# Performance work log

Hardware: AMD Instinct MI355X
Metric: run time of the kernel (lower is better)

The kernel has to match this reference:

```python
import jax, jax.numpy as jnp
import numpy as np

C0, C1 = 16, 16
V, E = 100000, 1600000
TWO_PI = 6.2831853


def setup_inputs() -> dict:
    key = jax.random.key(0)
    ks = jax.random.split(key, 12)
    s0 = 1.0 / np.sqrt(C0)
    s1 = 1.0 / np.sqrt(C1)
    return {
        "x": jax.random.normal(ks[0], (V, C0 + 2 * C1), dtype=jnp.float32),
        "edge_index": jax.random.randint(ks[1], (2, E), 0, V, dtype=jnp.int64),
        "angles": jax.random.uniform(ks[2], (E,), dtype=jnp.float32) * TWO_PI,
        "transporters": jax.random.uniform(ks[3], (E,), dtype=jnp.float32) * TWO_PI,
        "e1": jax.random.normal(ks[4], (V, 3), dtype=jnp.float32),
        "e2": jax.random.normal(ks[5], (V, 3), dtype=jnp.float32),
        # mag head (out rho0): self rho0->rho0, neigh rho0->rho0 (const), neigh rho1->rho0 (2 basis coeffs/chan)
        "w_self0": jax.random.normal(ks[6], (C0,), dtype=jnp.float32) * s0,
        "w_n00": jax.random.normal(ks[7], (C0,), dtype=jnp.float32) * s0,
        "w_n10": jax.random.normal(ks[8], (C1, 2), dtype=jnp.float32) * s1,
        # tangent head (out rho1): self rho1->rho1 {I,J}, neigh rho0->rho1 (2), neigh rho1->rho1 (4)
        "w_self11": jax.random.normal(ks[9], (C1, 2), dtype=jnp.float32) * s1,
        "w_n01": jax.random.normal(ks[10], (C0, 2), dtype=jnp.float32) * s0,
        "w_n11": jax.random.normal(ks[11], (C1, 4), dtype=jnp.float32) * s1,
    }


def _gem_head(x, edge_index, angles, transporters,
              w_self0, w_n00, w_n10, w_self11, w_n01, w_n11):
    """Gauge-equivariant message passing (GEM-CNN style).
    Returns (tangent_coeffs (V,2), mag (V,))."""
    nV = x.shape[0]
    x0 = x[:, :C0]                       # (V, C0) scalar (rho0) channels
    x1 = x[:, C0:].reshape(nV, C1, 2)    # (V, C1, 2) vector (rho1) channels
    src, dst = edge_index[0], edge_index[1]

    # gather + parallel transport of rho1 features (rotate by transporter angle g)
    cg, sg = jnp.cos(transporters)[:, None], jnp.sin(transporters)[:, None]
    x1s = x1[src]                        # (E, C1, 2)
    u1 = cg * x1s[..., 0] - sg * x1s[..., 1]
    u2 = sg * x1s[..., 0] + cg * x1s[..., 1]
    x0s = x0[src]                        # (E, C0)

    ct, st = jnp.cos(angles)[:, None], jnp.sin(angles)[:, None]
    c2t, s2t = jnp.cos(2.0 * angles)[:, None], jnp.sin(2.0 * angles)[:, None]

    # ---- rho0 output (magnitude) messages ----
    # rho0->rho0: constant kernel; rho1->rho0: basis (cos,sin) and (-sin,cos)
    m0 = x0s @ w_n00 \
        + (ct * u1 + st * u2) @ w_n10[:, 0] \
        + (-st * u1 + ct * u2) @ w_n10[:, 1]          # (E,)

    # ---- rho1 output (tangent) messages ----
    # rho0->rho1: K = a*(cos,sin)^T + b*(-sin,cos)^T
    sa = x0s @ w_n01[:, 0]
    sb = x0s @ w_n01[:, 1]
    mv1 = sa * ct[:, 0] - sb * st[:, 0]
    mv2 = sa * st[:, 0] + sb * ct[:, 0]
    # rho1->rho1: basis {I, J, Refl(2t), J*Refl(2t)}
    p, q, r, s = w_n11[:, 0], w_n11[:, 1], w_n11[:, 2], w_n11[:, 3]
    r1 = c2t * u1 + s2t * u2
    r2 = s2t * u1 - c2t * u2
    mv1 = mv1 + u1 @ p - u2 @ q + r1 @ r - r2 @ s
    mv2 = mv2 + u2 @ p + u1 @ q + r2 @ r + r1 @ s

    # ---- mean aggregation over incoming edges ----
    deg = jax.ops.segment_sum(jnp.ones_like(m0), dst, num_segments=nV)
    denom = jnp.maximum(deg, 1.0)
    mag = jax.ops.segment_sum(m0, dst, num_segments=nV) / denom
    agg1 = jax.ops.segment_sum(mv1, dst, num_segments=nV) / denom
    agg2 = jax.ops.segment_sum(mv2, dst, num_segments=nV) / denom

    # ---- self kernels (Schur-allowed blocks only) ----
    mag = mag + x0 @ w_self0
    sa_, sb_ = w_self11[:, 0], w_self11[:, 1]
    t1 = agg1 + x1[..., 0] @ sa_ - x1[..., 1] @ sb_
    t2 = agg2 + x1[..., 1] @ sa_ + x1[..., 0] @ sb_
    return jnp.stack([t1, t2], axis=-1), mag


def reference(x, edge_index, angles, transporters, e1, e2,
              w_self0, w_n00, w_n10, w_self11, w_n01, w_n11):
    tangent, mag = _gem_head(x, edge_index, angles, transporters,
                             w_self0, w_n00, w_n10, w_self11, w_n01, w_n11)
    mag_scale = jax.nn.sigmoid(mag)[:, None] * 2.0      # (V,1)
    wss_3d = tangent[:, 0:1] * e1 + tangent[:, 1:2] * e2  # (V,3)
    return wss_3d * mag_scale
```

## Files before the change

### kernel.cpp

```cpp
#include <hip/hip_runtime.h>
#include <math.h>


#define VB 256
#define VB_SHIFT 8
#define MAXNB 400
#define CHUNK 3125
#define NCHUNK 512
#define BIGT 1024
#define CAP_SHIFT 13
#define CAP (1 << CAP_SHIFT)
#define FIXS 131072.0f
#define FIXSI (1.0f / 131072.0f)
#define BIASI (1 << 22)

typedef unsigned int uint32;
typedef unsigned long long uint64;

static __device__ __forceinline__ uint32 f2bf(float f) {
    uint32 u = __float_as_uint(f);
    return (u + 0x7FFFu + ((u >> 16) & 1u)) >> 16;
}
static __device__ __forceinline__ uint32 pack2(float lo, float hi) {
    return f2bf(lo) | (f2bf(hi) << 16);
}
static __device__ __forceinline__ float bf_lo(uint32 u) {
    return __uint_as_float(u << 16);
}
static __device__ __forceinline__ float bf_hi(uint32 u) {
    return __uint_as_float(u & 0xFFFF0000u);
}

__global__ __launch_bounds__(256)
void precompute_kernel(const float* __restrict__ x,
                       const float* __restrict__ w_self0,
                       const float* __restrict__ w_n00,
                       const float* __restrict__ w_n10,
                       const float* __restrict__ w_self11,
                       const float* __restrict__ w_n01,
                       const float* __restrict__ w_n11,
                       uint32* __restrict__ table,
                       float* __restrict__ selfbuf,
                       int* __restrict__ fill,
                       int V, int NB) {
    __shared__ float stage[256 * 49];
    int tid = threadIdx.x;
    if (blockIdx.x == 0) {
        for (int i = tid; i < NB; i += 256) fill[i] = 0;
    }
    int v0 = blockIdx.x * 256;
    int nv = min(256, V - v0);
    if (nv <= 0) return;
    {
        const float4* x4 = (const float4*)(x + (size_t)v0 * 48);
        int n4 = nv * 12;
        for (int j = tid; j < n4; j += 256) {
            float4 f = x4[j];
            float* dp = stage + (j / 12) * 49 + (j % 12) * 4;
            dp[0] = f.x; dp[1] = f.y; dp[2] = f.z; dp[3] = f.w;
        }
    }
    __syncthreads();
    if (tid >= nv) return;
    int v = v0 + tid;
    const float* xr = stage + tid * 49;
    float d00 = 0.f, aw0 = 0.f, bw0 = 0.f, aw1 = 0.f, bw1 = 0.f;
    float d01a = 0.f, d01b = 0.f;
    float aP = 0.f, bP = 0.f, aQ = 0.f, bQ = 0.f;
    float aR = 0.f, bR = 0.f, aS = 0.f, bS = 0.f;
    float selfmag = 0.f, t1s = 0.f, t2s = 0.f;
#pragma unroll
    for (int i = 0; i < 16; ++i) {
        float x0 = xr[i];
        float a  = xr[16 + 2 * i];
        float b  = xr[17 + 2 * i];
        d00     += x0 * w_n00[i];
        selfmag += x0 * w_self0[i];
        d01a    += x0 * w_n01[i * 2 + 0];
        d01b    += x0 * w_n01[i * 2 + 1];
        float w0 = w_n10[i * 2 + 0], w1 = w_n10[i * 2 + 1];
        aw0 += a * w0;  bw0 += b * w0;
        aw1 += a * w1;  bw1 += b * w1;
        float p = w_n11[i * 4 + 0], q = w_n11[i * 4 + 1];
        float r = w_n11[i * 4 + 2], s = w_n11[i * 4 + 3];
        aP += a * p;  bP += b * p;
        aQ += a * q;  bQ += b * q;
        aR += a * r;  bR += b * r;
        aS += a * s;  bS += b * s;
        float sa_ = w_self11[i * 2 + 0], sb_ = w_self11[i * 2 + 1];
        t1s += a * sa_ - b * sb_;
        t2s += b * sa_ + a * sb_;
    }
    uint4 w0, w1;
    w0.x = pack2(d00, aw0);  w0.y = pack2(bw0, aw1);
    w0.z = pack2(bw1, d01a); w0.w = pack2(d01b, aP);
    w1.x = pack2(bP, aQ);    w1.y = pack2(bQ, aR);
    w1.z = pack2(bR, aS);    w1.w = pack2(bS, 0.f);
    uint4* tp = (uint4*)(table + (size_t)v * 8);
    tp[0] = w0;  tp[1] = w1;
    float* sf = selfbuf + (size_t)v * 4;
    sf[0] = selfmag; sf[1] = t1s; sf[2] = t2s; sf[3] = 0.f;
}

__global__ __launch_bounds__(BIGT)
void scatter_kernel(const int* __restrict__ src,
                    const int* __restrict__ dst,
                    const float* __restrict__ angles,
                    const float* __restrict__ transporters,
                    const uint32* __restrict__ table,
                    int* __restrict__ fill,
                    uint2* __restrict__ payload,
                    int E, int NB) {
    __shared__ int cnt_l[MAXNB];
    __shared__ int exoff_l[MAXNB];
    __shared__ int slot_l[MAXNB];
    __shared__ int wsum[16];
    __shared__ uint32 tw_src[CHUNK];
    __shared__ uint32 tw_ang[CHUNK];
    __shared__ uint32 tw_tr[CHUNK];
    __shared__ unsigned short tw_bin[CHUNK];

    int b = blockIdx.x;
    int lo = b * CHUNK;
    int hi = min(E, lo + CHUNK);
    int nloc = hi - lo;
    int tid = threadIdx.x;
    int lane = tid & 63;
    int wv = tid >> 6;

    for (int i = tid; i < NB; i += BIGT) cnt_l[i] = 0;
    __syncthreads();

    for (int e = lo + tid; e < hi; e += BIGT)
        atomicAdd(&cnt_l[dst[e] >> VB_SHIFT], 1);
    __syncthreads();

    int c = (tid < NB) ? cnt_l[tid] : 0;
    int rsv = 0;
    if (tid < NB && c > 0) rsv = atomicAdd(&fill[tid], c);

    int incl = c;
#pragma unroll
    for (int d = 1; d < 64; d <<= 1) {
        int n = __shfl_up(incl, d);
        if (lane >= d) incl += n;
    }
    if (lane == 63) wsum[wv] = incl;
    __syncthreads();
    if (tid < 16) {
        int wval = wsum[tid], winc = wval;
#pragma unroll
        for (int d = 1; d < 16; d <<= 1) {
            int n = __shfl_up(winc, d);
            if (lane >= d) winc += n;
        }
        wsum[tid] = winc - wval;
    }
    __syncthreads();
    if (tid < NB) {
        int ex = incl - c + wsum[wv];
        exoff_l[tid] = ex;
        cnt_l[tid] = ex;
        slot_l[tid] = (tid << CAP_SHIFT) + rsv;
    }
    __syncthreads();

    for (int e = lo + tid; e < hi; e += BIGT) {
        int d = dst[e];
        int bin = d >> VB_SHIFT;
        uint32 dl = (uint32)(d & (VB - 1));
        int pos = atomicAdd(&cnt_l[bin], 1);
        tw_src[pos] = (uint32)src[e] | (dl << 17);
        tw_ang[pos] = __float_as_uint(angles[e]);
        tw_tr[pos]  = __float_as_uint(transporters[e]);
        tw_bin[pos] = (unsigned short)bin;
    }
    __syncthreads();

    for (int k = tid; k < nloc; k += BIGT) {
        int bin = (int)tw_bin[k];
        uint32 w0i = tw_src[k];
        int s  = (int)(w0i & 0x1FFFFu);
        int dl = (int)(w0i >> 17);
        float ang = __uint_as_float(tw_ang[k]);
        float trv = __uint_as_float(tw_tr[k]);
        float st = __sinf(ang), ct = __cosf(ang);
        float sg = __sinf(trv), cg = __cosf(trv);
        float c2t = ct * ct - st * st;
        float s2t = 2.0f * st * ct;

        const uint4* tp = (const uint4*)(table + (size_t)s * 8);
        uint4 W0 = tp[0], W1 = tp[1];
        float d00 = bf_lo(W0.x), aw0 = bf_hi(W0.x);
        float bw0 = bf_lo(W0.y), aw1 = bf_hi(W0.y);
        float bw1 = bf_lo(W0.z), d01a = bf_hi(W0.z);
        float d01b = bf_lo(W0.w), aP = bf_hi(W0.w);
        float bP = bf_lo(W1.x), aQ = bf_hi(W1.x);
        float bQ = bf_lo(W1.y), aR = bf_hi(W1.y);
        float bR = bf_lo(W1.z), aS = bf_hi(W1.z);
        float bS = bf_lo(W1.w);

        float u1w0 = cg * aw0 - sg * bw0, u2w0 = sg * aw0 + cg * bw0;
        float u1w1 = cg * aw1 - sg * bw1, u2w1 = sg * aw1 + cg * bw1;
        float m0 = d00 + ct * u1w0 + st * u2w0 - st * u1w1 + ct * u2w1;

        float u1p = cg * aP - sg * bP, u2p = sg * aP + cg * bP;
        float u1q = cg * aQ - sg * bQ, u2q = sg * aQ + cg * bQ;
        float u1r = cg * aR - sg * bR, u2r = sg * aR + cg * bR;
        float u1s = cg * aS - sg * bS, u2s = sg * aS + cg * bS;

        float mv1 = d01a * ct - d01b * st
                  + u1p - u2q
                  + c2t * u1r + s2t * u2r
                  - (s2t * u1s - c2t * u2s);
        float mv2 = d01a * st + d01b * ct
                  + u2p + u1q
                  + s2t * u1r - c2t * u2r
                  + c2t * u1s + s2t * u2s;

        uint2 pl;
        pl.x = pack2(m0, mv1);
        pl.y = f2bf(mv2) | ((uint32)dl << 16);
        int g = slot_l[bin] + (k - exoff_l[bin]);
        if (g < ((bin + 1) << CAP_SHIFT))
            payload[g] = pl;
    }
}

__global__ __launch_bounds__(BIGT)
void bucket_kernel(const uint2* __restrict__ payload,
                   const int* __restrict__ fill,
                   const float* __restrict__ selfbuf,
                   const float* __restrict__ e1,
                   const float* __restrict__ e2,
                   float* __restrict__ out,
                   int V) {
    __shared__ uint64 acc[8][VB * 2];
    int bin = blockIdx.x;
    int tid = threadIdx.x;
    for (int i = tid; i < 8 * VB * 2; i += BIGT) ((uint64*)acc)[i] = 0ULL;
    __syncthreads();

    int n = min(fill[bin], CAP);
    const uint2* pp = payload + ((size_t)bin << CAP_SHIFT);
    uint64* myacc = acc[tid >> 7];
    for (int k = tid; k < n; k += BIGT) {
        uint2 pl = pp[k];
        float m0  = bf_lo(pl.x);
        float mv1 = bf_hi(pl.x);
        float mv2 = bf_lo(pl.y);
        int dl = (int)(pl.y >> 16);
        int m0f  = __float2int_rn(m0  * FIXS);
        int mv1f = __float2int_rn(mv1 * FIXS);
        int mv2f = __float2int_rn(mv2 * FIXS);
        uint64 pa = (uint64)(uint32)(m0f + BIASI)
                  | ((uint64)(uint32)mv1f << 32);
        uint64 pb = (uint64)(uint32)(mv2f + BIASI)
                  | (1ULL << 32);
        atomicAdd(&myacc[dl * 2 + 0], pa);
        atomicAdd(&myacc[dl * 2 + 1], pb);
    }
    __syncthreads();
    if (tid < VB) {
        int v = bin * VB + tid;
        if (v < V) {
            int cnt = 0, m0s = 0, mv1s = 0, mv2s = 0;
#pragma unroll
            for (int w = 0; w < 8; ++w) {
                uint64 a = acc[w][tid * 2 + 0];
                uint64 b = acc[w][tid * 2 + 1];
                uint32 nw = (uint32)(b >> 32);
                cnt  += (int)nw;
                m0s  += (int)((uint32)a - nw * (uint32)BIASI);
                mv1s += (int)(a >> 32);
                mv2s += (int)((uint32)b - nw * (uint32)BIASI);
            }
            float A0 = (float)m0s  * FIXSI;
            float A1 = (float)mv1s * FIXSI;
            float A2 = (float)mv2s * FIXSI;
            float inv = 1.0f / fmaxf((float)cnt, 1.0f);
            const float* sf = selfbuf + (size_t)v * 4;
            float mag = A0 * inv + sf[0];
            float t1  = A1 * inv + sf[1];
            float t2  = A2 * inv + sf[2];
            float scale = 2.0f / (1.0f + expf(-mag));
            float e1x = e1[v * 3 + 0], e1y = e1[v * 3 + 1], e1z = e1[v * 3 + 2];
            float e2x = e2[v * 3 + 0], e2y = e2[v * 3 + 1], e2z = e2[v * 3 + 2];
            out[v * 3 + 0] = (t1 * e1x + t2 * e2x) * scale;
            out[v * 3 + 1] = (t1 * e1y + t2 * e2y) * scale;
            out[v * 3 + 2] = (t1 * e1z + t2 * e2z) * scale;
        }
    }
}

extern "C" void kernel_launch(void* const* d_in, const int* in_sizes, int n_in,
                              void* d_out, int out_size, void* d_ws, size_t ws_size,
                              hipStream_t stream) {
    const float* x            = (const float*)d_in[0];
    const int*   edge_index   = (const int*)d_in[1];
    const float* angles       = (const float*)d_in[2];
    const float* transporters = (const float*)d_in[3];
    const float* e1           = (const float*)d_in[4];
    const float* e2           = (const float*)d_in[5];
    const float* w_self0      = (const float*)d_in[6];
    const float* w_n00        = (const float*)d_in[7];
    const float* w_n10        = (const float*)d_in[8];
    const float* w_self11     = (const float*)d_in[9];
    const float* w_n01        = (const float*)d_in[10];
    const float* w_n11        = (const float*)d_in[11];
    float* out = (float*)d_out;

    int V = in_sizes[0] / 48;
    int E = in_sizes[2];
    const int* src = edge_index;
    const int* dst = edge_index + E;

    int NB = (V + VB - 1) / VB;
    int nchunk = (E + CHUNK - 1) / CHUNK;

    char* p = (char*)d_ws;
    int* fill      = (int*)p;     p += (size_t)MAXNB * 4;
    uint32* table  = (uint32*)p;  p += (size_t)V * 8 * 4;
    float* selfbuf = (float*)p;   p += (size_t)V * 4 * 4;
    p = (char*)(((uintptr_t)p + 63) & ~(uintptr_t)63);
    uint2* payload = (uint2*)p;

    int gv = (V + 255) / 256;

    precompute_kernel<<<gv, 256, 0, stream>>>(
        x, w_self0, w_n00, w_n10, w_self11, w_n01, w_n11,
        table, selfbuf, fill, V, NB);
    scatter_kernel<<<nchunk, BIGT, 0, stream>>>(src, dst, angles,
                                                transporters, table,
                                                fill, payload, E, NB);
    bucket_kernel<<<NB, BIGT, 0, stream>>>(payload, fill, selfbuf,
                                           e1, e2, out, V);
}
```

Measured before the change: 138.3 us.

## Replace bucketed scatter with direct global 64-bit atomic accumulation per vertex

Removes the binning scatter kernel, the bf16 payload buffer and the LDS bucket reduction. Each edge now computes its message and does two packed fixed-point 64-bit atomicAdds straight into a per-vertex global accumulator, which precompute zeroes and a small finalize kernel reads. This drops the payload write/read round trip and the LDS sorting, at the cost of many contended global atomics over random destinations. It also removes the bf16 rounding of messages and the per-bin capacity limit.

```diff
diff --git a/kernel.cpp b/kernel.cpp
--- a/kernel.cpp
+++ b/kernel.cpp
@@ -2,14 +2,7 @@
 #include <math.h>
 
 
-#define VB 256
-#define VB_SHIFT 8
 #define MAXNB 400
-#define CHUNK 3125
-#define NCHUNK 512
-#define BIGT 1024
-#define CAP_SHIFT 13
-#define CAP (1 << CAP_SHIFT)
 #define FIXS 131072.0f
 #define FIXSI (1.0f / 131072.0f)
 #define BIASI (1 << 22)
@@ -41,16 +34,17 @@
                        const float* __restrict__ w_n11,
                        uint32* __restrict__ table,
                        float* __restrict__ selfbuf,
-                       int* __restrict__ fill,
-                       int V, int NB) {
+                       uint64* __restrict__ acc,
+                       int V) {
     __shared__ float stage[256 * 49];
     int tid = threadIdx.x;
-    if (blockIdx.x == 0) {
-        for (int i = tid; i < NB; i += 256) fill[i] = 0;
-    }
     int v0 = blockIdx.x * 256;
     int nv = min(256, V - v0);
     if (nv <= 0) return;
+    if (tid < nv) {
+        uint4 z = {0u, 0u, 0u, 0u};
+        *((uint4*)(acc + (size_t)(v0 + tid) * 2)) = z;
+    }
     {
         const float4* x4 = (const float4*)(x + (size_t)v0 * 48);
         int n4 = nv * 12;
@@ -102,88 +96,21 @@
     sf[0] = selfmag; sf[1] = t1s; sf[2] = t2s; sf[3] = 0.f;
 }
 
-__global__ __launch_bounds__(BIGT)
-void scatter_kernel(const int* __restrict__ src,
-                    const int* __restrict__ dst,
-                    const float* __restrict__ angles,
-                    const float* __restrict__ transporters,
-                    const uint32* __restrict__ table,
-                    int* __restrict__ fill,
-                    uint2* __restrict__ payload,
-                    int E, int NB) {
-    __shared__ int cnt_l[MAXNB];
-    __shared__ int exoff_l[MAXNB];
-    __shared__ int slot_l[MAXNB];
-    __shared__ int wsum[16];
-    __shared__ uint32 tw_src[CHUNK];
-    __shared__ uint32 tw_ang[CHUNK];
-    __shared__ uint32 tw_tr[CHUNK];
-    __shared__ unsigned short tw_bin[CHUNK];
-
-    int b = blockIdx.x;
-    int lo = b * CHUNK;
-    int hi = min(E, lo + CHUNK);
-    int nloc = hi - lo;
-    int tid = threadIdx.x;
-    int lane = tid & 63;
-    int wv = tid >> 6;
-
-    for (int i = tid; i < NB; i += BIGT) cnt_l[i] = 0;
-    __syncthreads();
-
-    for (int e = lo + tid; e < hi; e += BIGT)
-        atomicAdd(&cnt_l[dst[e] >> VB_SHIFT], 1);
-    __syncthreads();
-
-    int c = (tid < NB) ? cnt_l[tid] : 0;
-    int rsv = 0;
-    if (tid < NB && c > 0) rsv = atomicAdd(&fill[tid], c);
-
-    int incl = c;
-#pragma unroll
-    for (int d = 1; d < 64; d <<= 1) {
-        int n = __shfl_up(incl, d);
-        if (lane >= d) incl += n;
-    }
-    if (lane == 63) wsum[wv] = incl;
-    __syncthreads();
-    if (tid < 16) {
-        int wval = wsum[tid], winc = wval;
-#pragma unroll
-        for (int d = 1; d < 16; d <<= 1) {
-            int n = __shfl_up(winc, d);
-            if (lane >= d) winc += n;
-        }
-        wsum[tid] = winc - wval;
-    }
-    __syncthreads();
-    if (tid < NB) {
-        int ex = incl - c + wsum[wv];
-        exoff_l[tid] = ex;
-        cnt_l[tid] = ex;
-        slot_l[tid] = (tid << CAP_SHIFT) + rsv;
-    }
-    __syncthreads();
-
-    for (int e = lo + tid; e < hi; e += BIGT) {
+__global__ __launch_bounds__(256)
+void edge_kernel(const int* __restrict__ src,
+                 const int* __restrict__ dst,
+                 const float* __restrict__ angles,
+                 const float* __restrict__ transporters,
+                 const uint32* __restrict__ table,
+                 uint64* __restrict__ acc,
+                 int E) {
+    int i0 = blockIdx.x * 256 + threadIdx.x;
+    int stride = gridDim.x * 256;
+    for (int e = i0; e < E; e += stride) {
+        int s = src[e];
         int d = dst[e];
-        int bin = d >> VB_SHIFT;
-        uint32 dl = (uint32)(d & (VB - 1));
-        int pos = atomicAdd(&cnt_l[bin], 1);
-        tw_src[pos] = (uint32)src[e] | (dl << 17);
-        tw_ang[pos] = __float_as_uint(angles[e]);
-        tw_tr[pos]  = __float_as_uint(transporters[e]);
-        tw_bin[pos] = (unsigned short)bin;
-    }
-    __syncthreads();
-
-    for (int k = tid; k < nloc; k += BIGT) {
-        int bin = (int)tw_bin[k];
-        uint32 w0i = tw_src[k];
-        int s  = (int)(w0i & 0x1FFFFu);
-        int dl = (int)(w0i >> 17);
-        float ang = __uint_as_float(tw_ang[k]);
-        float trv = __uint_as_float(tw_tr[k]);
+        float ang = angles[e];
+        float trv = transporters[e];
         float st = __sinf(ang), ct = __cosf(ang);
         float sg = __sinf(trv), cg = __cosf(trv);
         float c2t = ct * ct - st * st;
@@ -218,38 +145,6 @@
                   + s2t * u1r - c2t * u2r
                   + c2t * u1s + s2t * u2s;
 
-        uint2 pl;
-        pl.x = pack2(m0, mv1);
-        pl.y = f2bf(mv2) | ((uint32)dl << 16);
-        int g = slot_l[bin] + (k - exoff_l[bin]);
-        if (g < ((bin + 1) << CAP_SHIFT))
-            payload[g] = pl;
-    }
-}
-
-__global__ __launch_bounds__(BIGT)
-void bucket_kernel(const uint2* __restrict__ payload,
-                   const int* __restrict__ fill,
-                   const float* __restrict__ selfbuf,
-                   const float* __restrict__ e1,
-                   const float* __restrict__ e2,
-                   float* __restrict__ out,
-                   int V) {
-    __shared__ uint64 acc[8][VB * 2];
-    int bin = blockIdx.x;
-    int tid = threadIdx.x;
-    for (int i = tid; i < 8 * VB * 2; i += BIGT) ((uint64*)acc)[i] = 0ULL;
-    __syncthreads();
-
-    int n = min(fill[bin], CAP);
-    const uint2* pp = payload + ((size_t)bin << CAP_SHIFT);
-    uint64* myacc = acc[tid >> 7];
-    for (int k = tid; k < n; k += BIGT) {
-        uint2 pl = pp[k];
-        float m0  = bf_lo(pl.x);
-        float mv1 = bf_hi(pl.x);
-        float mv2 = bf_lo(pl.y);
-        int dl = (int)(pl.y >> 16);
         int m0f  = __float2int_rn(m0  * FIXS);
         int mv1f = __float2int_rn(mv1 * FIXS);
         int mv2f = __float2int_rn(mv2 * FIXS);
@@ -257,40 +152,41 @@
                   | ((uint64)(uint32)mv1f << 32);
         uint64 pb = (uint64)(uint32)(mv2f + BIASI)
                   | (1ULL << 32);
-        atomicAdd(&myacc[dl * 2 + 0], pa);
-        atomicAdd(&myacc[dl * 2 + 1], pb);
-    }
-    __syncthreads();
-    if (tid < VB) {
-        int v = bin * VB + tid;
-        if (v < V) {
-            int cnt = 0, m0s = 0, mv1s = 0, mv2s = 0;
-#pragma unroll
-            for (int w = 0; w < 8; ++w) {
-                uint64 a = acc[w][tid * 2 + 0];
-                uint64 b = acc[w][tid * 2 + 1];
-                uint32 nw = (uint32)(b >> 32);
-                cnt  += (int)nw;
-                m0s  += (int)((uint32)a - nw * (uint32)BIASI);
-                mv1s += (int)(a >> 32);
-                mv2s += (int)((uint32)b - nw * (uint32)BIASI);
-            }
-            float A0 = (float)m0s  * FIXSI;
-            float A1 = (float)mv1s * FIXSI;
-            float A2 = (float)mv2s * FIXSI;
-            float inv = 1.0f / fmaxf((float)cnt, 1.0f);
-            const float* sf = selfbuf + (size_t)v * 4;
-            float mag = A0 * inv + sf[0];
-            float t1  = A1 * inv + sf[1];
-            float t2  = A2 * inv + sf[2];
-            float scale = 2.0f / (1.0f + expf(-mag));
-            float e1x = e1[v * 3 + 0], e1y = e1[v * 3 + 1], e1z = e1[v * 3 + 2];
-            float e2x = e2[v * 3 + 0], e2y = e2[v * 3 + 1], e2z = e2[v * 3 + 2];
-            out[v * 3 + 0] = (t1 * e1x + t2 * e2x) * scale;
-            out[v * 3 + 1] = (t1 * e1y + t2 * e2y) * scale;
-            out[v * 3 + 2] = (t1 * e1z + t2 * e2z) * scale;
-        }
-    }
+        atomicAdd(&acc[(size_t)d * 2 + 0], pa);
+        atomicAdd(&acc[(size_t)d * 2 + 1], pb);
+    }
+}
+
+__global__ __launch_bounds__(256)
+void finalize_kernel(const uint64* __restrict__ acc,
+                     const float* __restrict__ selfbuf,
+                     const float* __restrict__ e1,
+                     const float* __restrict__ e2,
+                     float* __restrict__ out,
+                     int V) {
+    int v = blockIdx.x * 256 + threadIdx.x;
+    if (v >= V) return;
+    uint64 a = acc[(size_t)v * 2 + 0];
+    uint64 b = acc[(size_t)v * 2 + 1];
+    uint32 nw = (uint32)(b >> 32);
+    int cnt  = (int)nw;
+    int m0s  = (int)((uint32)a - nw * (uint32)BIASI);
+    int mv1s = (int)(a >> 32);
+    int mv2s = (int)((uint32)b - nw * (uint32)BIASI);
+    float A0 = (float)m0s  * FIXSI;
+    float A1 = (float)mv1s * FIXSI;
+    float A2 = (float)mv2s * FIXSI;
+    float inv = 1.0f / fmaxf((float)cnt, 1.0f);
+    const float* sf = selfbuf + (size_t)v * 4;
+    float mag = A0 * inv + sf[0];
+    float t1  = A1 * inv + sf[1];
+    float t2  = A2 * inv + sf[2];
+    float scale = 2.0f / (1.0f + expf(-mag));
+    float e1x = e1[v * 3 + 0], e1y = e1[v * 3 + 1], e1z = e1[v * 3 + 2];
+    float e2x = e2[v * 3 + 0], e2y = e2[v * 3 + 1], e2z = e2[v * 3 + 2];
+    out[v * 3 + 0] = (t1 * e1x + t2 * e2x) * scale;
+    out[v * 3 + 1] = (t1 * e1y + t2 * e2y) * scale;
+    out[v * 3 + 2] = (t1 * e1z + t2 * e2z) * scale;
 }
 
 extern "C" void kernel_launch(void* const* d_in, const int* in_sizes, int n_in,
@@ -315,24 +211,19 @@
     const int* src = edge_index;
     const int* dst = edge_index + E;
 
-    int NB = (V + VB - 1) / VB;
-    int nchunk = (E + CHUNK - 1) / CHUNK;
-
     char* p = (char*)d_ws;
-    int* fill      = (int*)p;     p += (size_t)MAXNB * 4;
     uint32* table  = (uint32*)p;  p += (size_t)V * 8 * 4;
     float* selfbuf = (float*)p;   p += (size_t)V * 4 * 4;
     p = (char*)(((uintptr_t)p + 63) & ~(uintptr_t)63);
-    uint2* payload = (uint2*)p;
+    uint64* acc    = (uint64*)p;  p += (size_t)V * 2 * 8;
 
     int gv = (V + 255) / 256;
 
     precompute_kernel<<<gv, 256, 0, stream>>>(
         x, w_self0, w_n00, w_n10, w_self11, w_n01, w_n11,
-        table, selfbuf, fill, V, NB);
-    scatter_kernel<<<nchunk, BIGT, 0, stream>>>(src, dst, angles,
-                                                transporters, table,
-                                                fill, payload, E, NB);
-    bucket_kernel<<<NB, BIGT, 0, stream>>>(payload, fill, selfbuf,
-                                           e1, e2, out, V);
-}
+        table, selfbuf, acc, V);
+    int ge = min((E + 255) / 256, 2048);
+    edge_kernel<<<ge, 256, 0, stream>>>(src, dst, angles, transporters,
+                                        table, acc, E);
+    finalize_kernel<<<gv, 256, 0, stream>>>(acc, selfbuf, e1, e2, out, V);
+}
```

New measurement: 247.9 us. 79.2% more time.

## Simplify scatter: drop LDS staging and prefix scan, write payload via atomic cursors

Applied to the files above, without the earlier changes.

The scatter kernel no longer stages edges in LDS sorted by destination bin with a block-wide prefix scan. Each thread now reads its edge directly, takes its output slot from a per-bin LDS atomic cursor seeded from the global fill reservation, and computes the message in place. Chunk size and block size are halved to 1563 edges and 512 threads, giving more, smaller blocks. This removes several barriers, the scan and the LDS round trip. In exchange, payload writes within a bin are no longer contiguous by edge order, LDS atomics are contended, and edges are handled in original order rather than grouped by bin, which may hurt write coalescing.

```diff
diff --git a/kernel.cpp b/kernel.cpp
--- a/kernel.cpp
+++ b/kernel.cpp
@@ -5,8 +5,8 @@
 #define VB 256
 #define VB_SHIFT 8
 #define MAXNB 400
-#define CHUNK 3125
-#define NCHUNK 512
+#define CHUNK 1563
+#define ST 512
 #define BIGT 1024
 #define CAP_SHIFT 13
 #define CAP (1 << CAP_SHIFT)
@@ -46,7 +46,7 @@
     __shared__ float stage[256 * 49];
     int tid = threadIdx.x;
     if (blockIdx.x == 0) {
-        for (int i = tid; i < NB; i += 256) fill[i] = 0;
+        for (int i = tid; i < MAXNB; i += 256) fill[i] = 0;
     }
     int v0 = blockIdx.x * 256;
     int nv = min(256, V - v0);
@@ -102,7 +102,7 @@
     sf[0] = selfmag; sf[1] = t1s; sf[2] = t2s; sf[3] = 0.f;
 }
 
-__global__ __launch_bounds__(BIGT)
+__global__ __launch_bounds__(ST)
 void scatter_kernel(const int* __restrict__ src,
                     const int* __restrict__ dst,
                     const float* __restrict__ angles,
@@ -112,78 +112,35 @@
                     uint2* __restrict__ payload,
                     int E, int NB) {
     __shared__ int cnt_l[MAXNB];
-    __shared__ int exoff_l[MAXNB];
-    __shared__ int slot_l[MAXNB];
-    __shared__ int wsum[16];
-    __shared__ uint32 tw_src[CHUNK];
-    __shared__ uint32 tw_ang[CHUNK];
-    __shared__ uint32 tw_tr[CHUNK];
-    __shared__ unsigned short tw_bin[CHUNK];
 
     int b = blockIdx.x;
     int lo = b * CHUNK;
     int hi = min(E, lo + CHUNK);
-    int nloc = hi - lo;
     int tid = threadIdx.x;
-    int lane = tid & 63;
-    int wv = tid >> 6;
-
-    for (int i = tid; i < NB; i += BIGT) cnt_l[i] = 0;
-    __syncthreads();
-
-    for (int e = lo + tid; e < hi; e += BIGT)
+
+    for (int i = tid; i < NB; i += ST) cnt_l[i] = 0;
+    __syncthreads();
+
+    for (int e = lo + tid; e < hi; e += ST)
         atomicAdd(&cnt_l[dst[e] >> VB_SHIFT], 1);
     __syncthreads();
 
-    int c = (tid < NB) ? cnt_l[tid] : 0;
-    int rsv = 0;
-    if (tid < NB && c > 0) rsv = atomicAdd(&fill[tid], c);
-
-    int incl = c;
-#pragma unroll
-    for (int d = 1; d < 64; d <<= 1) {
-        int n = __shfl_up(incl, d);
-        if (lane >= d) incl += n;
-    }
-    if (lane == 63) wsum[wv] = incl;
-    __syncthreads();
-    if (tid < 16) {
-        int wval = wsum[tid], winc = wval;
-#pragma unroll
-        for (int d = 1; d < 16; d <<= 1) {
-            int n = __shfl_up(winc, d);
-            if (lane >= d) winc += n;
-        }
-        wsum[tid] = winc - wval;
-    }
-    __syncthreads();
     if (tid < NB) {
-        int ex = incl - c + wsum[wv];
-        exoff_l[tid] = ex;
-        cnt_l[tid] = ex;
-        slot_l[tid] = (tid << CAP_SHIFT) + rsv;
-    }
-    __syncthreads();
-
-    for (int e = lo + tid; e < hi; e += BIGT) {
+        int c = cnt_l[tid];
+        int rsv = (c > 0) ? atomicAdd(&fill[tid], c) : 0;
+        cnt_l[tid] = (tid << CAP_SHIFT) + rsv;
+    }
+    __syncthreads();
+
+    for (int e = lo + tid; e < hi; e += ST) {
         int d = dst[e];
         int bin = d >> VB_SHIFT;
-        uint32 dl = (uint32)(d & (VB - 1));
-        int pos = atomicAdd(&cnt_l[bin], 1);
-        tw_src[pos] = (uint32)src[e] | (dl << 17);
-        tw_ang[pos] = __float_as_uint(angles[e]);
-        tw_tr[pos]  = __float_as_uint(transporters[e]);
-        tw_bin[pos] = (unsigned short)bin;
-    }
-    __syncthreads();
-
-    for (int k = tid; k < nloc; k += BIGT) {
-        int bin = (int)tw_bin[k];
-        uint32 w0i = tw_src[k];
-        int s  = (int)(w0i & 0x1FFFFu);
-        int dl = (int)(w0i >> 17);
-        float ang = __uint_as_float(tw_ang[k]);
-        float trv = __uint_as_float(tw_tr[k]);
+        int dl = d & (VB - 1);
+        int s = src[e];
+        float ang = angles[e];
+        float trv = transporters[e];
+        int g = atomicAdd(&cnt_l[bin], 1);
+
         float st = __sinf(ang), ct = __cosf(ang);
         float sg = __sinf(trv), cg = __cosf(trv);
         float c2t = ct * ct - st * st;
@@ -221,7 +178,6 @@
         uint2 pl;
         pl.x = pack2(m0, mv1);
         pl.y = f2bf(mv2) | ((uint32)dl << 16);
-        int g = slot_l[bin] + (k - exoff_l[bin]);
         if (g < ((bin + 1) << CAP_SHIFT))
             payload[g] = pl;
     }
@@ -330,9 +286,9 @@
     precompute_kernel<<<gv, 256, 0, stream>>>(
         x, w_self0, w_n00, w_n10, w_self11, w_n01, w_n11,
         table, selfbuf, fill, V, NB);
-    scatter_kernel<<<nchunk, BIGT, 0, stream>>>(src, dst, angles,
-                                                transporters, table,
-                                                fill, payload, E, NB);
+    scatter_kernel<<<nchunk, ST, 0, stream>>>(src, dst, angles,
+                                              transporters, table,
+                                              fill, payload, E, NB);
     bucket_kernel<<<NB, BIGT, 0, stream>>>(payload, fill, selfbuf,
                                            e1, e2, out, V);
 }
```

After: 163.1 us. 1.18x slower.
